# Kernel optimization log

Measured on AMD Instinct MI355X. Metric: run time of the kernel, lower is better.

Reference implementation:

```python
import jax, jax.numpy as jnp
import numpy as np

INF = 1000000000000000.0  # 1e15, matches the TF source

B, H, S, D = 4, 16, 1024, 64


def setup_inputs() -> dict:
    key = jax.random.key(0)
    kq, kk, kv, kp = jax.random.split(key, 4)
    q = jax.random.normal(kq, (B, H, S, D), dtype=jnp.float32)
    k = jax.random.normal(kk, (B, H, S, D), dtype=jnp.float32)
    v = jax.random.normal(kv, (B, H, S, D), dtype=jnp.float32)
    # pad_mask: 1 = masked-out key position, broadcast over heads and queries
    pad_mask = jax.random.randint(kp, (B, 1, 1, S), 0, 2, dtype=jnp.int32)
    # look_ahead_mask: 1 above the diagonal (future positions masked)
    look_ahead_mask = jnp.triu(jnp.ones((S, S), dtype=jnp.int32), k=1)[None, None]
    return {"q": q, "k": k, "v": v, "pad_mask": pad_mask,
            "look_ahead_mask": look_ahead_mask}


def reference(q, k, v, pad_mask, look_ahead_mask):
    d_model = jnp.float32(q.shape[3])
    # scores: (B, H, Sq, Sk)
    score_logits = jnp.einsum("bhqd,bhkd->bhqk", q, k) / jnp.sqrt(d_model)
    if pad_mask is not None:
        score_logits = score_logits + pad_mask.astype(jnp.float32) * (-INF)
    if look_ahead_mask is not None:
        score_logits = score_logits + look_ahead_mask.astype(jnp.float32) * (-INF)
    attention_weights = jax.nn.softmax(score_logits, axis=-1)
    context_vector = jnp.einsum("bhqk,bhkd->bhqd", attention_weights, v)
    return (context_vector, attention_weights)
```

## Files before the change

### kernel.cpp

```cpp
#include <hip/hip_runtime.h>
#include <stdint.h>

#define S 1024
#define D 64
#define TQ 16
#define KT 128
#define NKT 8
#define NEG (-1e15f)
#define SCALE 0.125f

#define WB_STRIDE 1048
#define KB_STRIDE 72
#define VT_STRIDE 136
#define QS_STRIDE 72

typedef __bf16 bf16x8 __attribute__((ext_vector_type(8)));
typedef float f32x4 __attribute__((ext_vector_type(4)));
typedef unsigned short ushort_t;

__device__ __forceinline__ unsigned short f2b(float f) {
  union { float f; uint32_t u; } c; c.f = f;
  uint32_t u = c.u;
  return (unsigned short)((u + 0x7fffu + ((u >> 16) & 1u)) >> 16);
}
__device__ __forceinline__ float b2f(uint32_t u) {
  union { uint32_t u; float f; } c; c.u = u << 16;
  return c.f;
}

__global__ __launch_bounds__(256) void prep_k_kernel(
    const float* __restrict__ Kg, ushort_t* __restrict__ Kb)
{
  const size_t idx = ((size_t)blockIdx.x * 256 + threadIdx.x) * 8;
  float4 a = *(const float4*)(Kg + idx);
  float4 b = *(const float4*)(Kg + idx + 4);
  ushort_t tmp[8];
  tmp[0]=f2b(a.x); tmp[1]=f2b(a.y); tmp[2]=f2b(a.z); tmp[3]=f2b(a.w);
  tmp[4]=f2b(b.x); tmp[5]=f2b(b.y); tmp[6]=f2b(b.z); tmp[7]=f2b(b.w);
  *(uint4*)(Kb + idx) = *(const uint4*)tmp;
}

__global__ __launch_bounds__(256) void prep_vt_kernel(
    const float* __restrict__ Vg, ushort_t* __restrict__ Vt)
{
  __shared__ __align__(16) ushort_t lvt[D * QS_STRIDE];
  const int t = threadIdx.x;
  const int bh = blockIdx.x >> 4;
  const int j0 = (blockIdx.x & 15) << 6;

  {
    const int j = t >> 2, sd = (t & 3) << 4;
    const float* src = Vg + ((size_t)bh * S + j0 + j) * D + sd;
#pragma unroll
    for (int c = 0; c < 4; ++c) {
      float4 f = *(const float4*)(src + (c << 2));
      lvt[(sd + (c << 2) + 0) * QS_STRIDE + j] = f2b(f.x);
      lvt[(sd + (c << 2) + 1) * QS_STRIDE + j] = f2b(f.y);
      lvt[(sd + (c << 2) + 2) * QS_STRIDE + j] = f2b(f.z);
      lvt[(sd + (c << 2) + 3) * QS_STRIDE + j] = f2b(f.w);
    }
  }
  __syncthreads();
  {
    const int d = t >> 2, sj = (t & 3) << 4;
    ushort_t tmp[16];
#pragma unroll
    for (int c = 0; c < 4; ++c)
      *(ushort4*)&tmp[c << 2] = *(const ushort4*)&lvt[d * QS_STRIDE + sj + (c << 2)];
    ushort_t* dst = Vt + ((size_t)bh * D + d) * S + j0 + sj;
    *(uint4*)dst = *(const uint4*)&tmp[0];
    *(uint4*)(dst + 8) = *(const uint4*)&tmp[8];
  }
}

__global__ __launch_bounds__(512, 6) void attn_kernel(
    const float* __restrict__ Qg, const ushort_t* __restrict__ Kb,
    const ushort_t* __restrict__ Vtb, const int* __restrict__ PADg,
    float* __restrict__ OCTX, float* __restrict__ OW)
{
  __shared__ __align__(16) ushort_t wb[TQ * WB_STRIDE];
  __shared__ __align__(16) ushort_t ub[KT * KB_STRIDE];

  const int t  = threadIdx.x;
  const int w  = t >> 6;
  const int l  = t & 63;
  const int la = l & 15;
  const int lb = l >> 4;
  const int blk = blockIdx.x;
  const int bh  = blk >> 6;
  const int qt  = blk & 63;
  const int qr0 = qt << 4;

  const size_t head = (size_t)bh * S * D;
  const int* pp = PADg + (size_t)(bh >> 4) * S;

  bf16x8 aq0, aq1;
  {
    const float* qrow = Qg + head + (size_t)(qr0 + la) * D + (lb << 3);
    float4 q00 = *(const float4*)(qrow);
    float4 q01 = *(const float4*)(qrow + 4);
    float4 q10 = *(const float4*)(qrow + 32);
    float4 q11 = *(const float4*)(qrow + 36);
    ushort_t a0[8], a1[8];
    a0[0]=f2b(q00.x); a0[1]=f2b(q00.y); a0[2]=f2b(q00.z); a0[3]=f2b(q00.w);
    a0[4]=f2b(q01.x); a0[5]=f2b(q01.y); a0[6]=f2b(q01.z); a0[7]=f2b(q01.w);
    a1[0]=f2b(q10.x); a1[1]=f2b(q10.y); a1[2]=f2b(q10.z); a1[3]=f2b(q10.w);
    a1[4]=f2b(q11.x); a1[5]=f2b(q11.y); a1[6]=f2b(q11.z); a1[7]=f2b(q11.w);
    aq0 = *(const bf16x8*)a0;
    aq1 = *(const bf16x8*)a1;
  }

  for (int kt = 0; kt < NKT; ++kt) {
    {
      const ushort_t* kp = Kb + head + (size_t)(kt * KT) * D;
      const int row = t >> 2, off = (t & 3) << 4;
      const ushort_t* src = kp + row * D + off;
      ushort_t* dst = &ub[row * KB_STRIDE + off];
      *(uint4*)dst = *(const uint4*)src;
      *(uint4*)(dst + 8) = *(const uint4*)(src + 8);
    }
    __syncthreads();
    {
      const int j0 = w << 4;
      f32x4 acc = {0.f, 0.f, 0.f, 0.f};
      bf16x8 b0 = *(const bf16x8*)&ub[(j0 + la) * KB_STRIDE + (lb << 3)];
      acc = __builtin_amdgcn_mfma_f32_16x16x32_bf16(aq0, b0, acc, 0, 0, 0);
      bf16x8 b1 = *(const bf16x8*)&ub[(j0 + la) * KB_STRIDE + 32 + (lb << 3)];
      acc = __builtin_amdgcn_mfma_f32_16x16x32_bf16(aq1, b1, acc, 0, 0, 0);
#pragma unroll
      for (int i = 0; i < 4; ++i)
        wb[((lb << 2) + i) * WB_STRIDE + kt * KT + j0 + la] = f2b(acc[i]);
    }
    __syncthreads();
  }

#pragma unroll
  for (int rr = 0; rr < 2; ++rr) {
    const int r  = (w << 1) + rr;
    const int qr = qr0 + r;
    float lg[16];
    float m = -3.0e38f;
#pragma unroll
    for (int ii = 0; ii < 8; ++ii) {
      const int j = (l << 1) + (ii << 7);
      uint32_t pr = *(const uint32_t*)&wb[r * WB_STRIDE + j];
      int2 pv = *(const int2*)&pp[j];
      float l0 = b2f(pr & 0xffffu) * SCALE + (pv.x ? NEG : 0.0f) + ((j     > qr) ? NEG : 0.0f);
      float l1 = b2f(pr >> 16)     * SCALE + (pv.y ? NEG : 0.0f) + ((j + 1 > qr) ? NEG : 0.0f);
      lg[2 * ii] = l0; lg[2 * ii + 1] = l1;
      m = fmaxf(m, fmaxf(l0, l1));
    }
#pragma unroll
    for (int off = 32; off > 0; off >>= 1) m = fmaxf(m, __shfl_xor(m, off, 64));
    float sum = 0.f;
#pragma unroll
    for (int x = 0; x < 16; ++x) { lg[x] = __expf(lg[x] - m); sum += lg[x]; }
#pragma unroll
    for (int off = 32; off > 0; off >>= 1) sum += __shfl_xor(sum, off, 64);
    const float inv = 1.0f / sum;
    float* orow = OW + (size_t)(bh * S + qr) * S;
#pragma unroll
    for (int ii = 0; ii < 8; ++ii) {
      const int j = (l << 1) + (ii << 7);
      float w0 = lg[2 * ii] * inv, w1 = lg[2 * ii + 1] * inv;
      *(uint32_t*)&wb[r * WB_STRIDE + j] = ((uint32_t)f2b(w1) << 16) | (uint32_t)f2b(w0);
      *(float2*)&orow[j] = make_float2(w0, w1);
    }
  }
  __syncthreads();

  const int jh = w >> 2;
  const int d0 = (w & 3) << 4;
  f32x4 cacc = {0.f, 0.f, 0.f, 0.f};
  for (int kt = 0; kt < NKT; ++kt) {
    {
      const ushort_t* vp = Vtb + (size_t)bh * D * S + kt * KT;
      const int dd = t >> 3, off = (t & 7) << 4;
      const ushort_t* src = vp + (size_t)dd * S + off;
      ushort_t* dst = &ub[dd * VT_STRIDE + off];
      *(uint4*)dst = *(const uint4*)src;
      *(uint4*)(dst + 8) = *(const uint4*)(src + 8);
    }
    __syncthreads();
#pragma unroll
    for (int ks = 0; ks < 2; ++ks) {
      const int jt = jh * 64 + ks * 32;
      bf16x8 af = *(const bf16x8*)&wb[la * WB_STRIDE + kt * KT + jt + (lb << 3)];
      bf16x8 bf = *(const bf16x8*)&ub[(d0 + la) * VT_STRIDE + jt + (lb << 3)];
      cacc = __builtin_amdgcn_mfma_f32_16x16x32_bf16(af, bf, cacc, 0, 0, 0);
    }
    __syncthreads();
  }

  float* pbuf = (float*)ub;
  if (w >= 4) {
#pragma unroll
    for (int i = 0; i < 4; ++i)
      pbuf[(w - 4) * 320 + ((lb << 2) + i) * 20 + la] = cacc[i];
  }
  __syncthreads();
  if (w < 4) {
#pragma unroll
    for (int i = 0; i < 4; ++i) {
      const int qrow = (lb << 2) + i;
      OCTX[((size_t)(bh * S) + qr0 + qrow) * D + d0 + la] =
          cacc[i] + pbuf[w * 320 + qrow * 20 + la];
    }
  }
}

extern "C" void kernel_launch(void* const* d_in, const int* in_sizes, int n_in,
                              void* d_out, int out_size, void* d_ws, size_t ws_size,
                              hipStream_t stream) {
  const float* q   = (const float*)d_in[0];
  const float* k   = (const float*)d_in[1];
  const float* v   = (const float*)d_in[2];
  const int*   pad = (const int*)d_in[3];
  float* ctx  = (float*)d_out;
  float* wout = (float*)d_out + (size_t)4 * 16 * S * D;

  ushort_t* Kb  = (ushort_t*)d_ws;
  ushort_t* Vtb = (ushort_t*)d_ws + (size_t)4 * 16 * S * D;

  prep_k_kernel <<<dim3(2048), dim3(256), 0, stream>>>(k, Kb);
  prep_vt_kernel<<<dim3(1024), dim3(256), 0, stream>>>(v, Vtb);
  attn_kernel   <<<dim3(4096), dim3(512), 0, stream>>>(q, Kb, Vtb, pad, ctx, wout);
}
```

Measured before the change: 409.7 us.

## Load K and V tiles directly from global memory into MFMA operands, drop LDS staging

The K and V^T operands for both matrix multiplies are now read straight from global memory into registers instead of being staged through shared memory tile by tile. This removes the per-tile barriers and the K/V shared buffer, shrinking LDS use so the occupancy hint rises from 6 to 8 blocks. Each wave now covers a contiguous 128-key range for QK and a 512-key half for PV. The softmax pass is widened to 4-element vector loads and stores. The trade-off is uncoalesced 16-byte global reads per lane that lean on cache hits instead of shared-memory reuse.

```diff
diff --git a/kernel.cpp b/kernel.cpp
--- a/kernel.cpp
+++ b/kernel.cpp
@@ -4,14 +4,10 @@
 #define S 1024
 #define D 64
 #define TQ 16
-#define KT 128
-#define NKT 8
 #define NEG (-1e15f)
 #define SCALE 0.125f
 
 #define WB_STRIDE 1048
-#define KB_STRIDE 72
-#define VT_STRIDE 136
 #define QS_STRIDE 72
 
 typedef __bf16 bf16x8 __attribute__((ext_vector_type(8)));
@@ -73,13 +69,13 @@
   }
 }
 
-__global__ __launch_bounds__(512, 6) void attn_kernel(
+__global__ __launch_bounds__(512, 8) void attn_kernel(
     const float* __restrict__ Qg, const ushort_t* __restrict__ Kb,
     const ushort_t* __restrict__ Vtb, const int* __restrict__ PADg,
     float* __restrict__ OCTX, float* __restrict__ OW)
 {
   __shared__ __align__(16) ushort_t wb[TQ * WB_STRIDE];
-  __shared__ __align__(16) ushort_t ub[KT * KB_STRIDE];
+  __shared__ __align__(16) float pbuf[4 * 16 * 20];
 
   const int t  = threadIdx.x;
   const int w  = t >> 6;
@@ -110,29 +106,23 @@
     aq1 = *(const bf16x8*)a1;
   }
 
-  for (int kt = 0; kt < NKT; ++kt) {
-    {
-      const ushort_t* kp = Kb + head + (size_t)(kt * KT) * D;
-      const int row = t >> 2, off = (t & 3) << 4;
-      const ushort_t* src = kp + row * D + off;
-      ushort_t* dst = &ub[row * KB_STRIDE + off];
-      *(uint4*)dst = *(const uint4*)src;
-      *(uint4*)(dst + 8) = *(const uint4*)(src + 8);
-    }
-    __syncthreads();
-    {
-      const int j0 = w << 4;
+  {
+    const ushort_t* kbase = Kb + head;
+#pragma unroll
+    for (int s = 0; s < 8; ++s) {
+      const int j0 = (w << 7) + (s << 4);
+      const ushort_t* krow = kbase + (size_t)(j0 + la) * D + (lb << 3);
       f32x4 acc = {0.f, 0.f, 0.f, 0.f};
-      bf16x8 b0 = *(const bf16x8*)&ub[(j0 + la) * KB_STRIDE + (lb << 3)];
+      bf16x8 b0 = *(const bf16x8*)(krow);
+      bf16x8 b1 = *(const bf16x8*)(krow + 32);
       acc = __builtin_amdgcn_mfma_f32_16x16x32_bf16(aq0, b0, acc, 0, 0, 0);
-      bf16x8 b1 = *(const bf16x8*)&ub[(j0 + la) * KB_STRIDE + 32 + (lb << 3)];
       acc = __builtin_amdgcn_mfma_f32_16x16x32_bf16(aq1, b1, acc, 0, 0, 0);
 #pragma unroll
       for (int i = 0; i < 4; ++i)
-        wb[((lb << 2) + i) * WB_STRIDE + kt * KT + j0 + la] = f2b(acc[i]);
-    }
-    __syncthreads();
-  }
+        wb[((lb << 2) + i) * WB_STRIDE + j0 + la] = f2b(acc[i]);
+    }
+  }
+  __syncthreads();
 
 #pragma unroll
   for (int rr = 0; rr < 2; ++rr) {
@@ -141,14 +131,16 @@
     float lg[16];
     float m = -3.0e38f;
 #pragma unroll
-    for (int ii = 0; ii < 8; ++ii) {
-      const int j = (l << 1) + (ii << 7);
-      uint32_t pr = *(const uint32_t*)&wb[r * WB_STRIDE + j];
-      int2 pv = *(const int2*)&pp[j];
-      float l0 = b2f(pr & 0xffffu) * SCALE + (pv.x ? NEG : 0.0f) + ((j     > qr) ? NEG : 0.0f);
-      float l1 = b2f(pr >> 16)     * SCALE + (pv.y ? NEG : 0.0f) + ((j + 1 > qr) ? NEG : 0.0f);
-      lg[2 * ii] = l0; lg[2 * ii + 1] = l1;
-      m = fmaxf(m, fmaxf(l0, l1));
+    for (int ii = 0; ii < 4; ++ii) {
+      const int j = (l << 2) + (ii << 8);
+      uint2 pr = *(const uint2*)&wb[r * WB_STRIDE + j];
+      int4 pv = *(const int4*)&pp[j];
+      float l0 = b2f(pr.x & 0xffffu) * SCALE + (pv.x ? NEG : 0.0f) + ((j     > qr) ? NEG : 0.0f);
+      float l1 = b2f(pr.x >> 16)     * SCALE + (pv.y ? NEG : 0.0f) + ((j + 1 > qr) ? NEG : 0.0f);
+      float l2 = b2f(pr.y & 0xffffu) * SCALE + (pv.z ? NEG : 0.0f) + ((j + 2 > qr) ? NEG : 0.0f);
+      float l3 = b2f(pr.y >> 16)     * SCALE + (pv.w ? NEG : 0.0f) + ((j + 3 > qr) ? NEG : 0.0f);
+      lg[4*ii] = l0; lg[4*ii+1] = l1; lg[4*ii+2] = l2; lg[4*ii+3] = l3;
+      m = fmaxf(m, fmaxf(fmaxf(l0, l1), fmaxf(l2, l3)));
     }
 #pragma unroll
     for (int off = 32; off > 0; off >>= 1) m = fmaxf(m, __shfl_xor(m, off, 64));
@@ -160,11 +152,15 @@
     const float inv = 1.0f / sum;
     float* orow = OW + (size_t)(bh * S + qr) * S;
 #pragma unroll
-    for (int ii = 0; ii < 8; ++ii) {
-      const int j = (l << 1) + (ii << 7);
-      float w0 = lg[2 * ii] * inv, w1 = lg[2 * ii + 1] * inv;
-      *(uint32_t*)&wb[r * WB_STRIDE + j] = ((uint32_t)f2b(w1) << 16) | (uint32_t)f2b(w0);
-      *(float2*)&orow[j] = make_float2(w0, w1);
+    for (int ii = 0; ii < 4; ++ii) {
+      const int j = (l << 2) + (ii << 8);
+      float w0 = lg[4*ii] * inv, w1 = lg[4*ii+1] * inv;
+      float w2 = lg[4*ii+2] * inv, w3 = lg[4*ii+3] * inv;
+      uint2 pk;
+      pk.x = ((uint32_t)f2b(w1) << 16) | (uint32_t)f2b(w0);
+      pk.y = ((uint32_t)f2b(w3) << 16) | (uint32_t)f2b(w2);
+      *(uint2*)&wb[r * WB_STRIDE + j] = pk;
+      *(float4*)&orow[j] = make_float4(w0, w1, w2, w3);
     }
   }
   __syncthreads();
@@ -172,27 +168,17 @@
   const int jh = w >> 2;
   const int d0 = (w & 3) << 4;
   f32x4 cacc = {0.f, 0.f, 0.f, 0.f};
-  for (int kt = 0; kt < NKT; ++kt) {
-    {
-      const ushort_t* vp = Vtb + (size_t)bh * D * S + kt * KT;
-      const int dd = t >> 3, off = (t & 7) << 4;
-      const ushort_t* src = vp + (size_t)dd * S + off;
-      ushort_t* dst = &ub[dd * VT_STRIDE + off];
-      *(uint4*)dst = *(const uint4*)src;
-      *(uint4*)(dst + 8) = *(const uint4*)(src + 8);
-    }
-    __syncthreads();
-#pragma unroll
-    for (int ks = 0; ks < 2; ++ks) {
-      const int jt = jh * 64 + ks * 32;
-      bf16x8 af = *(const bf16x8*)&wb[la * WB_STRIDE + kt * KT + jt + (lb << 3)];
-      bf16x8 bf = *(const bf16x8*)&ub[(d0 + la) * VT_STRIDE + jt + (lb << 3)];
+  {
+    const ushort_t* vbase = Vtb + (size_t)bh * D * S + (size_t)(d0 + la) * S;
+#pragma unroll
+    for (int ks = 0; ks < 16; ++ks) {
+      const int jt = (jh << 9) + (ks << 5);
+      bf16x8 af = *(const bf16x8*)&wb[la * WB_STRIDE + jt + (lb << 3)];
+      bf16x8 bf = *(const bf16x8*)(vbase + jt + (lb << 3));
       cacc = __builtin_amdgcn_mfma_f32_16x16x32_bf16(af, bf, cacc, 0, 0, 0);
     }
-    __syncthreads();
-  }
-
-  float* pbuf = (float*)ub;
+  }
+
   if (w >= 4) {
 #pragma unroll
     for (int i = 0; i < 4; ++i)
```

Measured after the change: 459.2 us. +12.1%, slower.
